# Kernel optimization log

Hardware: AMD Instinct MI355X
Metric: run time of the kernel (lower is better)

## Reference

```python
import jax, jax.numpy as jnp
import numpy as np

T, B, I, H = 2048, 128, 256, 256


def setup_inputs() -> dict:
    key = jax.random.key(0)
    k = jax.random.split(key, 6)
    stdv = 1.0 / np.sqrt(H)
    return {
        "x": jax.random.normal(k[0], (T, B, I), dtype=jnp.float32),
        "h0": jax.random.normal(k[1], (1, B, H), dtype=jnp.float32),
        "w_ih": jax.random.uniform(k[2], (3 * H, I), jnp.float32, -stdv, stdv),
        "w_hh": jax.random.uniform(k[3], (3 * H, H), jnp.float32, -stdv, stdv),
        "b_ih": jax.random.uniform(k[4], (3 * H,), jnp.float32, -stdv, stdv),
        "b_hh": jax.random.uniform(k[5], (3 * H,), jnp.float32, -stdv, stdv),
    }


def _gru_scan(x, h0, w_ih, w_hh, b_ih, b_hh):
    # Precompute input projections for all timesteps: [T, B, 3H]
    gi = jnp.einsum('tbi,gi->tbg', x, w_ih) + b_ih
    hdim = w_hh.shape[1]

    def step(h, gi_t):
        gh = h @ w_hh.T + b_hh  # [B, 3H]
        i_r, i_z, i_n = jnp.split(gi_t, 3, axis=-1)
        h_r, h_z, h_n = jnp.split(gh, 3, axis=-1)
        r = jax.nn.sigmoid(i_r + h_r)
        z = jax.nn.sigmoid(i_z + h_z)
        n = jnp.tanh(i_n + r * h_n)
        h_new = (1.0 - z) * n + z * h
        return h_new, h_new

    h_last, outs = jax.lax.scan(step, h0, gi)
    return outs, h_last


def reference(x, h0, w_ih, w_hh, b_ih, b_hh):
    # x: [T, B, I] (seq-major, batch_first=False); h0: [1, B, H]
    outs, h_last = _gru_scan(x, h0[0], w_ih, w_hh, b_ih, b_hh)
    return outs, h_last[None]  # ([T,B,H], [1,B,H])
```

## Files before the change

kernel.cpp:

```cpp
#include <hip/hip_runtime.h>
#include <stdint.h>


#define T_SEQ 2048
#define BATCH 128
#define IDIM  256
#define HDIM  256
#define G3    768

typedef float f32x4 __attribute__((ext_vector_type(4)));
typedef short bf16x8 __attribute__((ext_vector_type(8)));

__device__ __forceinline__ uint16_t f2bf(float f) {
  union { float f; uint32_t u; } v; v.f = f;
  uint32_t u = v.u;
  return (uint16_t)((u + 0x7fffu + ((u >> 16) & 1u)) >> 16);
}
__device__ __forceinline__ uint32_t pack2(float a, float b) {
  return (uint32_t)f2bf(a) | ((uint32_t)f2bf(b) << 16);
}
__device__ __forceinline__ float bf2f(uint16_t h) {
  union { uint32_t u; float f; } v; v.u = ((uint32_t)h) << 16;
  return v.f;
}
__device__ __forceinline__ float dot2bf(uint32_t w, uint32_t h, float acc) {
#if defined(__has_builtin)
#if __has_builtin(__builtin_amdgcn_fdot2_f32_bf16)
  typedef __bf16 v2bf __attribute__((ext_vector_type(2)));
  union U { uint32_t u; v2bf v; };
  U a, b; a.u = w; b.u = h;
  return __builtin_amdgcn_fdot2_f32_bf16(a.v, b.v, acc, false);
#else
  asm("v_dot2_f32_bf16 %0, %1, %2, %0" : "+v"(acc) : "v"(w), "v"(h));
  return acc;
#endif
#else
  asm("v_dot2_f32_bf16 %0, %1, %2, %0" : "+v"(acc) : "v"(w), "v"(h));
  return acc;
#endif
}

#define GEMM_NT 6
#define GEMM_KS 8
#define LDSROW  1552

__global__ __launch_bounds__(512, 2)
void gi_gemm(const float* __restrict__ x, const float* __restrict__ w_ih,
             const float* __restrict__ b_ih, uint16_t* __restrict__ gi,
             int tiles) {
  __shared__ __align__(16) uint8_t lds_raw[16 * LDSROW];
  const int tid  = threadIdx.x;
  const int lane = tid & 63;
  const int wv   = tid >> 6;
  const int l15  = lane & 15;
  const int lk   = lane >> 4;

  bf16x8 bfrag[GEMM_NT][GEMM_KS];
  float  bias[GEMM_NT];
#pragma unroll
  for (int nt = 0; nt < GEMM_NT; ++nt) {
    const int col = wv * 96 + nt * 16 + l15;
    bias[nt] = b_ih[col];
#pragma unroll
    for (int ks = 0; ks < GEMM_KS; ++ks) {
      const int kb = ks * 32 + lk * 8;
      const float4* p = (const float4*)(w_ih + (size_t)col * IDIM + kb);
      float4 w0 = p[0], w1 = p[1];
      union { uint32_t u[4]; bf16x8 v; } pk;
      pk.u[0] = pack2(w0.x, w0.y); pk.u[1] = pack2(w0.z, w0.w);
      pk.u[2] = pack2(w1.x, w1.y); pk.u[3] = pack2(w1.z, w1.w);
      bfrag[nt][ks] = pk.v;
    }
  }

  for (int tile = blockIdx.x; tile < tiles; tile += gridDim.x) {
    const int m0 = tile * 16;
    f32x4 acc[GEMM_NT];
#pragma unroll
    for (int nt = 0; nt < GEMM_NT; ++nt) {
      f32x4 z = {0.f, 0.f, 0.f, 0.f};
      acc[nt] = z;
    }
#pragma unroll
    for (int ks = 0; ks < GEMM_KS; ++ks) {
      const float4* p = (const float4*)(x + (size_t)(m0 + l15) * IDIM + ks * 32 + lk * 8);
      float4 a0 = p[0], a1 = p[1];
      union { uint32_t u[4]; bf16x8 v; } pk;
      pk.u[0] = pack2(a0.x, a0.y); pk.u[1] = pack2(a0.z, a0.w);
      pk.u[2] = pack2(a1.x, a1.y); pk.u[3] = pack2(a1.z, a1.w);
#pragma unroll
      for (int nt = 0; nt < GEMM_NT; ++nt)
        acc[nt] = __builtin_amdgcn_mfma_f32_16x16x32_bf16(pk.v, bfrag[nt][ks], acc[nt], 0, 0, 0);
    }
#pragma unroll
    for (int nt = 0; nt < GEMM_NT; ++nt) {
      const int col = wv * 96 + nt * 16 + l15;
#pragma unroll
      for (int i = 0; i < 4; ++i) {
        const int row = lk * 4 + i;
        *(uint16_t*)(lds_raw + row * LDSROW + col * 2) = f2bf(acc[nt][i] + bias[nt]);
      }
    }
    __syncthreads();
    {
      const int row = tid >> 5, c = tid & 31;
      const uint4* src = (const uint4*)(lds_raw + row * LDSROW + c * 48);
      uint4* dst = (uint4*)((uint8_t*)gi + (size_t)(m0 + row) * G3 * 2 + c * 48);
      dst[0] = src[0]; dst[1] = src[1]; dst[2] = src[2];
    }
    __syncthreads();
  }
}

__global__ __launch_bounds__(512, 2)
void gru_scan(const uint16_t* __restrict__ gi, const float* __restrict__ w_hh,
              const float* __restrict__ b_hh, const float* __restrict__ h0,
              float* __restrict__ hstate, float* __restrict__ out,
              int t0, int cT) {
  __shared__ __align__(16) uint4 hbuf4[32];
  __shared__ float part[G3 * 2];
  const int b   = blockIdx.x;
  const int tid = threadIdx.x;
  const int j   = tid & 255;
  const int q   = tid >> 8;

  uint32_t wr[64], wz[64], wn[64];
#pragma unroll
  for (int p = 0; p < 64; ++p) {
    float2 a = ((const float2*)(w_hh + (size_t)(0 * 256 + j) * HDIM + q * 128))[p];
    float2 c = ((const float2*)(w_hh + (size_t)(1 * 256 + j) * HDIM + q * 128))[p];
    float2 d = ((const float2*)(w_hh + (size_t)(2 * 256 + j) * HDIM + q * 128))[p];
    wr[p] = pack2(a.x, a.y);
    wz[p] = pack2(c.x, c.y);
    wn[p] = pack2(d.x, d.y);
  }
  const float bhr = b_hh[j], bhz = b_hh[256 + j], bhn = b_hh[512 + j];

  float h = 0.f;
  if (q == 0) {
    h = (t0 == 0) ? h0[b * HDIM + j] : hstate[b * HDIM + j];
    ((uint16_t*)hbuf4)[j] = f2bf(h);
  }
  __syncthreads();

  const uint16_t* gib = gi + (size_t)b * G3 + j;
  float gr = 0.f, gz = 0.f, gn = 0.f;
  if (q == 0) {
    const uint16_t* p = gib;
    gr = bf2f(p[0]); gz = bf2f(p[256]); gn = bf2f(p[512]);
  }

  for (int tt = 0; tt < cT; ++tt) {
    float ar = 0.f, az = 0.f, an = 0.f;
#pragma unroll
    for (int p16 = 0; p16 < 16; ++p16) {
      uint4 hv = hbuf4[q * 16 + p16];
      ar = dot2bf(wr[p16 * 4 + 0], hv.x, ar);
      az = dot2bf(wz[p16 * 4 + 0], hv.x, az);
      an = dot2bf(wn[p16 * 4 + 0], hv.x, an);
      ar = dot2bf(wr[p16 * 4 + 1], hv.y, ar);
      az = dot2bf(wz[p16 * 4 + 1], hv.y, az);
      an = dot2bf(wn[p16 * 4 + 1], hv.y, an);
      ar = dot2bf(wr[p16 * 4 + 2], hv.z, ar);
      az = dot2bf(wz[p16 * 4 + 2], hv.z, az);
      an = dot2bf(wn[p16 * 4 + 2], hv.z, an);
      ar = dot2bf(wr[p16 * 4 + 3], hv.w, ar);
      az = dot2bf(wz[p16 * 4 + 3], hv.w, az);
      an = dot2bf(wn[p16 * 4 + 3], hv.w, an);
    }
    part[(0 * 256 + j) * 2 + q] = ar;
    part[(1 * 256 + j) * 2 + q] = az;
    part[(2 * 256 + j) * 2 + q] = an;
    __syncthreads();
    if (q == 0) {
      float2 pr = *(const float2*)&part[(0 * 256 + j) * 2];
      float2 pz = *(const float2*)&part[(1 * 256 + j) * 2];
      float2 pn = *(const float2*)&part[(2 * 256 + j) * 2];
      float sr = gr + pr.x + pr.y + bhr;
      float sz = gz + pz.x + pz.y + bhz;
      float hn = pn.x + pn.y + bhn;
      float r = 1.f / (1.f + __expf(-sr));
      float z = 1.f / (1.f + __expf(-sz));
      float xn = gn + r * hn;
      float e = __expf(-2.f * xn);
      float n = 1.f - 2.f * e / (1.f + e);
      h = (1.f - z) * n + z * h;
      out[((size_t)(t0 + tt) * BATCH + b) * HDIM + j] = h;
      ((uint16_t*)hbuf4)[j] = f2bf(h);
      if (tt + 1 < cT) {
        const uint16_t* p = gib + (size_t)(tt + 1) * BATCH * G3;
        gr = bf2f(p[0]); gz = bf2f(p[256]); gn = bf2f(p[512]);
      }
    }
    __syncthreads();
  }

  if (q == 0) {
    hstate[b * HDIM + j] = h;
    if (t0 + cT == T_SEQ)
      out[(size_t)T_SEQ * BATCH * HDIM + (size_t)b * HDIM + j] = h;
  }
}

extern "C" void kernel_launch(void* const* d_in, const int* in_sizes, int n_in,
                              void* d_out, int out_size, void* d_ws, size_t ws_size,
                              hipStream_t stream) {
  const float* x    = (const float*)d_in[0];
  const float* h0   = (const float*)d_in[1];
  const float* w_ih = (const float*)d_in[2];
  const float* w_hh = (const float*)d_in[3];
  const float* b_ih = (const float*)d_in[4];
  const float* b_hh = (const float*)d_in[5];
  float* out = (float*)d_out;

  const size_t HST = 1 << 17;
  float* hstate = (float*)d_ws;
  uint16_t* gi = (uint16_t*)((char*)d_ws + HST);

  const size_t per_t = (size_t)BATCH * G3 * 2;
  size_t cap = (ws_size > HST) ? (ws_size - HST) / per_t : 0;
  int chunk = (int)((cap < (size_t)T_SEQ) ? cap : (size_t)T_SEQ);
  if (chunk < 1) chunk = 1;

  for (int t0 = 0; t0 < T_SEQ; t0 += chunk) {
    const int cT = (T_SEQ - t0 < chunk) ? (T_SEQ - t0) : chunk;
    const int tiles = cT * BATCH / 16;
    gi_gemm<<<256, 512, 0, stream>>>(x + (size_t)t0 * BATCH * IDIM, w_ih, b_ih, gi, tiles);
    gru_scan<<<128, 512, 0, stream>>>(gi, w_hh, b_hh, h0, hstate, out, t0, cT);
  }
}
```

Baseline: 3.591 ms.

## Pair K-split lanes with shuffle reduction and double-buffer hidden state

Remaps threads so the two K-halves for a hidden unit sit in adjacent lanes. Their partial dot products are then combined with __shfl_xor instead of a shared-memory partial buffer, which removes one __syncthreads per timestep. The hidden state is double-buffered in LDS so the next step can be written without a second barrier. The next timestep's gi values are loaded before the dot products to hide their latency. Both lanes now compute the gate math redundantly, and the weight-load access pattern changes with the new thread mapping.

```diff
diff --git a/kernel.cpp b/kernel.cpp
--- a/kernel.cpp
+++ b/kernel.cpp
@@ -117,12 +117,14 @@
               const float* __restrict__ b_hh, const float* __restrict__ h0,
               float* __restrict__ hstate, float* __restrict__ out,
               int t0, int cT) {
-  __shared__ __align__(16) uint4 hbuf4[32];
-  __shared__ float part[G3 * 2];
+  __shared__ __align__(16) uint4 hbuf[2][32];
   const int b   = blockIdx.x;
   const int tid = threadIdx.x;
-  const int j   = tid & 255;
-  const int q   = tid >> 8;
+  const int j   = tid >> 1;
+  const int q   = tid & 1;
+
+  const uint16_t* gib = gi + (size_t)b * G3 + j;
+  float gr = bf2f(gib[0]), gz = bf2f(gib[256]), gn = bf2f(gib[512]);
 
   uint32_t wr[64], wz[64], wn[64];
 #pragma unroll
@@ -136,62 +138,58 @@
   }
   const float bhr = b_hh[j], bhz = b_hh[256 + j], bhn = b_hh[512 + j];
 
-  float h = 0.f;
-  if (q == 0) {
-    h = (t0 == 0) ? h0[b * HDIM + j] : hstate[b * HDIM + j];
-    ((uint16_t*)hbuf4)[j] = f2bf(h);
-  }
+  float h = (t0 == 0) ? h0[b * HDIM + j] : hstate[b * HDIM + j];
+  if (q == 0) ((uint16_t*)&hbuf[0][0])[j] = f2bf(h);
   __syncthreads();
 
-  const uint16_t* gib = gi + (size_t)b * G3 + j;
-  float gr = 0.f, gz = 0.f, gn = 0.f;
-  if (q == 0) {
-    const uint16_t* p = gib;
-    gr = bf2f(p[0]); gz = bf2f(p[256]); gn = bf2f(p[512]);
-  }
+  float* outp = out + (size_t)t0 * BATCH * HDIM + (size_t)b * HDIM + j;
 
   for (int tt = 0; tt < cT; ++tt) {
+    const int cur = tt & 1;
+    uint4 hv[16];
+#pragma unroll
+    for (int p = 0; p < 16; ++p) hv[p] = hbuf[cur][(q << 4) + p];
+    float grn = 0.f, gzn = 0.f, gnn = 0.f;
+    if (tt + 1 < cT) {
+      const uint16_t* p2 = gib + (size_t)(tt + 1) * BATCH * G3;
+      grn = bf2f(p2[0]); gzn = bf2f(p2[256]); gnn = bf2f(p2[512]);
+    }
+
     float ar = 0.f, az = 0.f, an = 0.f;
 #pragma unroll
-    for (int p16 = 0; p16 < 16; ++p16) {
-      uint4 hv = hbuf4[q * 16 + p16];
-      ar = dot2bf(wr[p16 * 4 + 0], hv.x, ar);
-      az = dot2bf(wz[p16 * 4 + 0], hv.x, az);
-      an = dot2bf(wn[p16 * 4 + 0], hv.x, an);
-      ar = dot2bf(wr[p16 * 4 + 1], hv.y, ar);
-      az = dot2bf(wz[p16 * 4 + 1], hv.y, az);
-      an = dot2bf(wn[p16 * 4 + 1], hv.y, an);
-      ar = dot2bf(wr[p16 * 4 + 2], hv.z, ar);
-      az = dot2bf(wz[p16 * 4 + 2], hv.z, az);
-      an = dot2bf(wn[p16 * 4 + 2], hv.z, an);
-      ar = dot2bf(wr[p16 * 4 + 3], hv.w, ar);
-      az = dot2bf(wz[p16 * 4 + 3], hv.w, az);
-      an = dot2bf(wn[p16 * 4 + 3], hv.w, an);
-    }
-    part[(0 * 256 + j) * 2 + q] = ar;
-    part[(1 * 256 + j) * 2 + q] = az;
-    part[(2 * 256 + j) * 2 + q] = an;
-    __syncthreads();
+    for (int p = 0; p < 16; ++p) {
+      ar = dot2bf(wr[p * 4 + 0], hv[p].x, ar);
+      az = dot2bf(wz[p * 4 + 0], hv[p].x, az);
+      an = dot2bf(wn[p * 4 + 0], hv[p].x, an);
+      ar = dot2bf(wr[p * 4 + 1], hv[p].y, ar);
+      az = dot2bf(wz[p * 4 + 1], hv[p].y, az);
+      an = dot2bf(wn[p * 4 + 1], hv[p].y, an);
+      ar = dot2bf(wr[p * 4 + 2], hv[p].z, ar);
+      az = dot2bf(wz[p * 4 + 2], hv[p].z, az);
+      an = dot2bf(wn[p * 4 + 2], hv[p].z, an);
+      ar = dot2bf(wr[p * 4 + 3], hv[p].w, ar);
+      az = dot2bf(wz[p * 4 + 3], hv[p].w, az);
+      an = dot2bf(wn[p * 4 + 3], hv[p].w, an);
+    }
+    ar += __shfl_xor(ar, 1);
+    az += __shfl_xor(az, 1);
+    an += __shfl_xor(an, 1);
+
+    float sr = gr + ar + bhr;
+    float sz = gz + az + bhz;
+    float hn = an + bhn;
+    float r = 1.f / (1.f + __expf(-sr));
+    float z = 1.f / (1.f + __expf(-sz));
+    float xn = gn + r * hn;
+    float e = __expf(-2.f * xn);
+    float n = 1.f - 2.f * e / (1.f + e);
+    h = (1.f - z) * n + z * h;
+
     if (q == 0) {
-      float2 pr = *(const float2*)&part[(0 * 256 + j) * 2];
-      float2 pz = *(const float2*)&part[(1 * 256 + j) * 2];
-      float2 pn = *(const float2*)&part[(2 * 256 + j) * 2];
-      float sr = gr + pr.x + pr.y + bhr;
-      float sz = gz + pz.x + pz.y + bhz;
-      float hn = pn.x + pn.y + bhn;
-      float r = 1.f / (1.f + __expf(-sr));
-      float z = 1.f / (1.f + __expf(-sz));
-      float xn = gn + r * hn;
-      float e = __expf(-2.f * xn);
-      float n = 1.f - 2.f * e / (1.f + e);
-      h = (1.f - z) * n + z * h;
-      out[((size_t)(t0 + tt) * BATCH + b) * HDIM + j] = h;
-      ((uint16_t*)hbuf4)[j] = f2bf(h);
-      if (tt + 1 < cT) {
-        const uint16_t* p = gib + (size_t)(tt + 1) * BATCH * G3;
-        gr = bf2f(p[0]); gz = bf2f(p[256]); gn = bf2f(p[512]);
-      }
-    }
+      outp[(size_t)tt * BATCH * HDIM] = h;
+      ((uint16_t*)&hbuf[cur ^ 1][0])[j] = f2bf(h);
+    }
+    gr = grn; gz = gzn; gn = gnn;
     __syncthreads();
   }
 
```

New measurement: 7.073 ms. 1.97x slower.
